# Performance work log

Measured on AMD Instinct MI355X. Metric: run time of the kernel, lower is better.

Reference implementation:

```python
import jax, jax.numpy as jnp
import numpy as np

N_HEAD = 16  # matches init_kwargs
LN_EPS = 1e-5


def setup_inputs() -> dict:
    key = jax.random.key(0)
    k0, k1, k2 = jax.random.split(key, 3)
    S, B, D = 2048, 2, 1024
    N, Dh = N_HEAD, D // N_HEAD
    h = jax.random.normal(k0, (S, B, D), dtype=jnp.float32)
    # causal mask, True = masked; source's dim==3 branch: shape [qlen, klen, batch]
    causal = jnp.triu(jnp.ones((S, S), dtype=bool), k=1)
    attn_mask = jnp.broadcast_to(causal[:, :, None], (S, S, B))
    W_qkv = jax.random.normal(k1, (D, 3 * N * Dh), dtype=jnp.float32) * (1.0 / np.sqrt(D))
    W_o = jax.random.normal(k2, (N * Dh, D), dtype=jnp.float32) * (1.0 / np.sqrt(N * Dh))
    gamma = jnp.ones((D,), dtype=jnp.float32)
    beta = jnp.zeros((D,), dtype=jnp.float32)
    return {"h": h, "attn_mask": attn_mask, "W_qkv": W_qkv, "W_o": W_o,
            "gamma": gamma, "beta": beta}


def reference(h, attn_mask, W_qkv, W_o, gamma, beta):
    # h: [S, B, D] (seq, batch, d_model) -- Transformer-XL layout
    S, B, D = h.shape
    N = N_HEAD
    Dh = W_o.shape[0] // N
    scale = 1.0 / np.sqrt(Dh)

    qkv = h @ W_qkv                                   # [S, B, 3*N*Dh]
    q, k, v = jnp.split(qkv, 3, axis=-1)
    q = q.reshape(S, B, N, Dh)
    k = k.reshape(S, B, N, Dh)
    v = v.reshape(S, B, N, Dh)

    # attention scores: [i, j, b, n]
    score = jnp.einsum('ibnd,jbnd->ijbn', q, k) * scale
    # mask (dim==3 branch of source): attn_mask [i, j, b] -> [i, j, b, 1]
    score = jnp.where(attn_mask[:, :, :, None], -jnp.inf, score)
    prob = jax.nn.softmax(score, axis=1)              # softmax over key axis j

    attn_vec = jnp.einsum('ijbn,jbnd->ibnd', prob, v).reshape(S, B, N * Dh)
    attn_out = attn_vec @ W_o                         # [S, B, D]

    # residual + LayerNorm (biased variance, like torch.nn.LayerNorm)
    x = h + attn_out
    mu = jnp.mean(x, axis=-1, keepdims=True)
    var = jnp.mean(jnp.square(x - mu), axis=-1, keepdims=True)
    out = (x - mu) * jax.lax.rsqrt(var + LN_EPS) * gamma + beta
    return out
```

## Files before the change

kernel.cpp:

```cpp
#include <hip/hip_runtime.h>

typedef unsigned short u16;
typedef unsigned int u32;
typedef __attribute__((ext_vector_type(8))) __bf16 bf16x8;
typedef __attribute__((ext_vector_type(4))) float f32x4;
typedef __attribute__((ext_vector_type(8))) unsigned short u16x8;
typedef __attribute__((ext_vector_type(4))) unsigned short u16x4;
typedef __attribute__((ext_vector_type(2))) unsigned int u32x2;
typedef __attribute__((ext_vector_type(4))) unsigned int u32x4;

#if defined(__has_builtin)
#if __has_builtin(__builtin_amdgcn_permlane32_swap) && __has_builtin(__builtin_amdgcn_permlane16_swap)
#define USE_PERMLANE 1
#endif
#endif
#ifndef USE_PERMLANE
#define USE_PERMLANE 0
#endif

__device__ __forceinline__ u16 f2bf(float f) {
    u32 u = __builtin_bit_cast(u32, f);
    u += 0x7fffu + ((u >> 16) & 1u);
    return (u16)(u >> 16);
}

__device__ __forceinline__ float fexp2(float x) {
#if __has_builtin(__builtin_amdgcn_exp2f)
    return __builtin_amdgcn_exp2f(x);
#else
    return exp2f(x);
#endif
}

__device__ __forceinline__ float frcp(float x) {
#if __has_builtin(__builtin_amdgcn_rcpf)
    return __builtin_amdgcn_rcpf(x);
#else
    return 1.0f / x;
#endif
}

__global__ __launch_bounds__(256) void conv_h_kernel(const float* __restrict__ h,
                                                     u16* __restrict__ hb) {
    int i = blockIdx.x * 256 + threadIdx.x;
    float4 v = ((const float4*)h)[i];
    u16x4 o = { f2bf(v.x), f2bf(v.y), f2bf(v.z), f2bf(v.w) };
    ((u16x4*)hb)[i] = o;
}

__global__ __launch_bounds__(256) void conv_wt_kernel(const float* __restrict__ W,
                                                      u16* __restrict__ Wt,
                                                      int R, int C,
                                                      int scale_rows, float scale) {
    __shared__ float tile[32][33];
    int t = threadIdx.x;
    int r = t >> 3, c4 = (t & 7) * 4;
    int gx = blockIdx.x * 32, gy = blockIdx.y * 32;
    float4 v = *(const float4*)&W[(size_t)(gy + r) * C + gx + c4];
    tile[r][c4 + 0] = v.x; tile[r][c4 + 1] = v.y;
    tile[r][c4 + 2] = v.z; tile[r][c4 + 3] = v.w;
    __syncthreads();
    float sc = (gx + r < scale_rows) ? scale : 1.0f;
    u16x4 o = { f2bf(tile[c4 + 0][r] * sc), f2bf(tile[c4 + 1][r] * sc),
                f2bf(tile[c4 + 2][r] * sc), f2bf(tile[c4 + 3][r] * sc) };
    *(u16x4*)&Wt[(size_t)(gx + r) * R + gy + c4] = o;
}

template <int MODE>
__global__ __launch_bounds__(256) void gemm_bt_kernel(
        const u16* __restrict__ A, const u16* __restrict__ Bt,
        u16* __restrict__ Cb, const float* __restrict__ H, float* __restrict__ X,
        int M, int N, int K) {
    constexpr int LDT = 40;
    __shared__ u16 alds[2][128 * LDT];
    __shared__ u16 blds[2][128 * LDT];
    const int t = threadIdx.x;
    const int lane = t & 63;
    const int wave = t >> 6;
    const int wm = wave >> 1, wn = wave & 1;
    const int m0 = blockIdx.x * 128;
    const int n0 = blockIdx.y * 128;
    const int nk = K >> 5;

    const int srow = t >> 1;
    const int sch = (t & 1) * 2;
    const u16* ga = A + (size_t)(m0 + srow) * K + sch * 8;
    const u16* gb = Bt + (size_t)(n0 + srow) * K + sch * 8;
    const int wo = srow * LDT + sch * 8;

    u16x8 ra0 = *(const u16x8*)(ga);
    u16x8 ra1 = *(const u16x8*)(ga + 8);
    u16x8 rb0 = *(const u16x8*)(gb);
    u16x8 rb1 = *(const u16x8*)(gb + 8);
    *(u16x8*)&alds[0][wo] = ra0;  *(u16x8*)&alds[0][wo + 8] = ra1;
    *(u16x8*)&blds[0][wo] = rb0;  *(u16x8*)&blds[0][wo + 8] = rb1;

    f32x4 acc[4][4] = {};
    const int ko = (lane >> 4) * 8;
    const int arow_base = wm * 64 + (lane & 15);
    const int brow_base = wn * 64 + (lane & 15);

    int cur = 0;
    for (int kt = 0; kt < nk; ++kt) {
        __syncthreads();
        if (kt + 1 < nk) {
            const u16* gan = ga + (kt + 1) * 32;
            const u16* gbn = gb + (kt + 1) * 32;
            ra0 = *(const u16x8*)(gan);
            ra1 = *(const u16x8*)(gan + 8);
            rb0 = *(const u16x8*)(gbn);
            rb1 = *(const u16x8*)(gbn + 8);
        }
        bf16x8 afrag[4], bfrag[4];
#pragma unroll
        for (int m = 0; m < 4; ++m)
            afrag[m] = *(const bf16x8*)&alds[cur][(arow_base + m * 16) * LDT + ko];
#pragma unroll
        for (int n = 0; n < 4; ++n)
            bfrag[n] = *(const bf16x8*)&blds[cur][(brow_base + n * 16) * LDT + ko];
#pragma unroll
        for (int m = 0; m < 4; ++m)
#pragma unroll
            for (int n = 0; n < 4; ++n)
                acc[m][n] = __builtin_amdgcn_mfma_f32_16x16x32_bf16(afrag[m], bfrag[n],
                                                                   acc[m][n], 0, 0, 0);
        if (kt + 1 < nk) {
            *(u16x8*)&alds[cur ^ 1][wo] = ra0;  *(u16x8*)&alds[cur ^ 1][wo + 8] = ra1;
            *(u16x8*)&blds[cur ^ 1][wo] = rb0;  *(u16x8*)&blds[cur ^ 1][wo + 8] = rb1;
        }
        cur ^= 1;
    }

#pragma unroll
    for (int m = 0; m < 4; ++m)
#pragma unroll
        for (int n = 0; n < 4; ++n)
#pragma unroll
            for (int r = 0; r < 4; ++r) {
                int row = m0 + wm * 64 + m * 16 + (lane >> 4) * 4 + r;
                int col = n0 + wn * 64 + n * 16 + (lane & 15);
                size_t idx = (size_t)row * N + col;
                if (MODE == 0) Cb[idx] = f2bf(acc[m][n][r]);
                else           X[idx] = acc[m][n][r] + H[idx];
            }
}

__global__ __launch_bounds__(256) void transpose_v_kernel(const u16* __restrict__ qkvb,
                                                          u16* __restrict__ vt) {
    __shared__ u16 tl[64][72];
    const int t = threadIdx.x;
    const int p = blockIdx.y;
    const int nn = p >> 1, b = p & 1;
    const int s0 = blockIdx.x * 64;
    const int r = t >> 2;
    const int ch = (t & 3) * 2;
    const u16* g = qkvb + ((size_t)(s0 + r) * 2 + b) * 3072 + 2048 + nn * 64;
    *(u16x8*)&tl[r][ch * 8]     = *(const u16x8*)(g + ch * 8);
    *(u16x8*)&tl[r][ch * 8 + 8] = *(const u16x8*)(g + ch * 8 + 8);
    __syncthreads();
    const int dh = t >> 2;
    const int sc = (t & 3) * 2;
    u16* o = vt + ((size_t)p * 64 + dh) * 2048 + s0;
#pragma unroll
    for (int q = 0; q < 2; ++q) {
        int scq = sc + q;
        u16x8 v;
#pragma unroll
        for (int j = 0; j < 8; ++j) v[j] = tl[scq * 8 + j][dh];
        *(u16x8*)(o + scq * 8) = v;
    }
}

__global__ __launch_bounds__(256) void attn_kernel(const u16* __restrict__ qkvb,
                                                   const u16* __restrict__ vt,
                                                   u16* __restrict__ attnb) {
    constexpr int LKT = 72;
    __shared__ u16 klds[2][64 * LKT];
    __shared__ u16 vlds[2][64 * LKT];
#if !USE_PERMLANE
    __shared__ u16 plds[4][16 * LKT];
#endif
    const int t = threadIdx.x;
    const int lane = t & 63;
    const int w = t >> 6;
    const int bid = blockIdx.x;
    const int g = bid >> 5;
    const int sq = g & 7, jq = g >> 3;
    const int qt = (jq == 0) ? (31 - sq) : (jq == 1) ? (16 + sq)
                 : (jq == 2) ? (15 - sq) : sq;
    const int p = bid & 31;
    const int nn = p >> 1, b = p & 1;
    const int i0 = qt * 64;

    const int li = lane & 15;
    const int lg = lane >> 4;

    const int qrow = i0 + w * 16 + li;
    const u16* qg = qkvb + ((size_t)qrow * 2 + b) * 3072 + nn * 64 + lg * 8;
    bf16x8 qa0 = *(const bf16x8*)(qg);
    bf16x8 qa1 = *(const bf16x8*)(qg + 32);

    f32x4 o[4] = {};
    float mrun = -3.0e38f;
    float lrun = 0.f;

    const int srow = t >> 2;
    const int sch = (t & 3) * 2;
    const u16* kg = qkvb + 1024 + nn * 64 + sch * 8;
    const u16* vg = vt + ((size_t)p * 64 + srow) * 2048 + sch * 8;
    const int swo = srow * LKT + sch * 8;

    const int nt = qt + 1;
    u16x8 k0, k1, v0, v1;
    {
        const u16* kgp = kg + ((size_t)srow * 2 + b) * 3072;
        k0 = *(const u16x8*)(kgp);  k1 = *(const u16x8*)(kgp + 8);
        v0 = *(const u16x8*)(vg);   v1 = *(const u16x8*)(vg + 8);
    }
    *(u16x8*)&klds[0][swo] = k0;  *(u16x8*)&klds[0][swo + 8] = k1;
    *(u16x8*)&vlds[0][swo] = v0;  *(u16x8*)&vlds[0][swo + 8] = v1;
    __syncthreads();

    for (int jt = 0; jt < nt; ++jt) {
        const int buf = jt & 1;
        if (jt + 1 < nt) {
            const u16* kgp = kg + ((size_t)(jt * 64 + 64 + srow) * 2 + b) * 3072;
            k0 = *(const u16x8*)(kgp);  k1 = *(const u16x8*)(kgp + 8);
            const u16* vgp = vg + jt * 64 + 64;
            v0 = *(const u16x8*)(vgp);  v1 = *(const u16x8*)(vgp + 8);
        }

        f32x4 st[4];
        __builtin_amdgcn_s_setprio(1);
#pragma unroll
        for (int cf = 0; cf < 4; ++cf) {
            bf16x8 kb0 = *(const bf16x8*)&klds[buf][(cf * 16 + li) * LKT + lg * 8];
            bf16x8 kb1 = *(const bf16x8*)&klds[buf][(cf * 16 + li) * LKT + 32 + lg * 8];
            f32x4 z = {};
            z = __builtin_amdgcn_mfma_f32_16x16x32_bf16(kb0, qa0, z, 0, 0, 0);
            z = __builtin_amdgcn_mfma_f32_16x16x32_bf16(kb1, qa1, z, 0, 0, 0);
            st[cf] = z;
        }
        __builtin_amdgcn_s_setprio(0);

        if (jt == qt) {
            const int it = w * 16 + li;
#pragma unroll
            for (int cf = 0; cf < 4; ++cf)
#pragma unroll
                for (int r = 0; r < 4; ++r) {
                    int jl = cf * 16 + lg * 4 + r;
                    if (jl > it) st[cf][r] = -3.0e38f;
                }
        }

        float mloc = st[0][0];
#pragma unroll
        for (int cf = 0; cf < 4; ++cf)
#pragma unroll
            for (int r = 0; r < 4; ++r) mloc = fmaxf(mloc, st[cf][r]);
        mloc = fmaxf(mloc, __shfl_xor(mloc, 16, 64));
        mloc = fmaxf(mloc, __shfl_xor(mloc, 32, 64));

        if (__any(mloc > mrun + 8.0f)) {
            float mnew = fmaxf(mrun, mloc);
            float alpha = fexp2(mrun - mnew);
            lrun *= alpha;
            mrun = mnew;
#pragma unroll
            for (int r = 0; r < 4; ++r) {
                float ar = __shfl(alpha, lg * 4 + r, 64);
#pragma unroll
                for (int cf = 0; cf < 4; ++cf) o[cf][r] *= ar;
            }
        }

#if USE_PERMLANE
        float rsum = 0.f;
        u32 wv[4][2];
#pragma unroll
        for (int cf = 0; cf < 4; ++cf)
#pragma unroll
            for (int rr = 0; rr < 2; ++rr) {
                float p0 = fexp2(st[cf][2 * rr] - mrun);
                float p1 = fexp2(st[cf][2 * rr + 1] - mrun);
                rsum += p0 + p1;
                u32 wres;
                asm("v_cvt_pk_bf16_f32 %0, %1, %2" : "=v"(wres) : "v"(p0), "v"(p1));
                wv[cf][rr] = wres;
            }
        rsum += __shfl_xor(rsum, 16, 64);
        rsum += __shfl_xor(rsum, 32, 64);
        lrun += rsum;

        __builtin_amdgcn_s_setprio(1);
#pragma unroll
        for (int ks = 0; ks < 2; ++ks) {
            u32x2 sa = __builtin_amdgcn_permlane32_swap(wv[2 * ks][0], wv[2 * ks + 1][0], false, false);
            u32x2 fa = __builtin_amdgcn_permlane16_swap(sa[0], sa[1], false, false);
            u32x2 sb = __builtin_amdgcn_permlane32_swap(wv[2 * ks][1], wv[2 * ks + 1][1], false, false);
            u32x2 fb = __builtin_amdgcn_permlane16_swap(sb[0], sb[1], false, false);
            u32x4 fw = { fa[0], fb[0], fa[1], fb[1] };
            bf16x8 pa = __builtin_bit_cast(bf16x8, fw);
#pragma unroll
            for (int cf = 0; cf < 4; ++cf) {
                bf16x8 vb = *(const bf16x8*)&vlds[buf][(cf * 16 + li) * LKT + ks * 32 + lg * 8];
                o[cf] = __builtin_amdgcn_mfma_f32_16x16x32_bf16(pa, vb, o[cf], 0, 0, 0);
            }
        }
        __builtin_amdgcn_s_setprio(0);
#else
        float rsum = 0.f;
#pragma unroll
        for (int cf = 0; cf < 4; ++cf) {
            u16x4 pw;
#pragma unroll
            for (int r = 0; r < 4; ++r) {
                float pv = fexp2(st[cf][r] - mrun);
                rsum += pv;
                pw[r] = f2bf(pv);
            }
            *(u16x4*)&plds[w][li * LKT + cf * 16 + lg * 4] = pw;
        }
        rsum += __shfl_xor(rsum, 16, 64);
        rsum += __shfl_xor(rsum, 32, 64);
        lrun += rsum;

        asm volatile("s_waitcnt lgkmcnt(0)" ::: "memory");
        __builtin_amdgcn_sched_barrier(0);

#pragma unroll
        for (int ks = 0; ks < 2; ++ks) {
            bf16x8 pa = *(const bf16x8*)&plds[w][li * LKT + ks * 32 + lg * 8];
#pragma unroll
            for (int cf = 0; cf < 4; ++cf) {
                bf16x8 vb = *(const bf16x8*)&vlds[buf][(cf * 16 + li) * LKT + ks * 32 + lg * 8];
                o[cf] = __builtin_amdgcn_mfma_f32_16x16x32_bf16(pa, vb, o[cf], 0, 0, 0);
            }
        }
#endif

        if (jt + 1 < nt) {
            *(u16x8*)&klds[buf ^ 1][swo] = k0;  *(u16x8*)&klds[buf ^ 1][swo + 8] = k1;
            *(u16x8*)&vlds[buf ^ 1][swo] = v0;  *(u16x8*)&vlds[buf ^ 1][swo + 8] = v1;
        }
        __syncthreads();
    }

    float rinv = frcp(lrun);
#pragma unroll
    for (int r = 0; r < 4; ++r) {
        float rv = __shfl(rinv, lg * 4 + r, 64);
        int srowg = i0 + w * 16 + lg * 4 + r;
        u16* og = attnb + ((size_t)srowg * 2 + b) * 1024 + nn * 64;
#pragma unroll
        for (int cf = 0; cf < 4; ++cf)
            og[cf * 16 + li] = f2bf(o[cf][r] * rv);
    }
}

__global__ __launch_bounds__(256) void ln_kernel(const float* __restrict__ X,
                                                 const float* __restrict__ gamma,
                                                 const float* __restrict__ beta,
                                                 float* __restrict__ out) {
    __shared__ float red[8];
    const int t = threadIdx.x;
    const int row = blockIdx.x;
    float4 v = ((const float4*)(X + (size_t)row * 1024))[t];
    float s = v.x + v.y + v.z + v.w;
#pragma unroll
    for (int off = 1; off < 64; off <<= 1) s += __shfl_xor(s, off, 64);
    if ((t & 63) == 0) red[t >> 6] = s;
    __syncthreads();
    float mu = (red[0] + red[1] + red[2] + red[3]) * (1.f / 1024.f);
    float dx = v.x - mu, dy = v.y - mu, dz = v.z - mu, dw = v.w - mu;
    float q = dx * dx + dy * dy + dz * dz + dw * dw;
#pragma unroll
    for (int off = 1; off < 64; off <<= 1) q += __shfl_xor(q, off, 64);
    if ((t & 63) == 0) red[4 + (t >> 6)] = q;
    __syncthreads();
    float var = (red[4] + red[5] + red[6] + red[7]) * (1.f / 1024.f);
    float rs = rsqrtf(var + 1e-5f);
    float4 g = ((const float4*)gamma)[t];
    float4 bt = ((const float4*)beta)[t];
    float4 o;
    o.x = dx * rs * g.x + bt.x;
    o.y = dy * rs * g.y + bt.y;
    o.z = dz * rs * g.z + bt.z;
    o.w = dw * rs * g.w + bt.w;
    ((float4*)(out + (size_t)row * 1024))[t] = o;
}

extern "C" void kernel_launch(void* const* d_in, const int* in_sizes, int n_in,
                              void* d_out, int out_size, void* d_ws, size_t ws_size,
                              hipStream_t stream) {
    const float* h     = (const float*)d_in[0];
    const float* Wqkv  = (const float*)d_in[2];
    const float* Wo    = (const float*)d_in[3];
    const float* gamma = (const float*)d_in[4];
    const float* beta  = (const float*)d_in[5];
    float* out = (float*)d_out;

    char* ws = (char*)d_ws;
    u16*   hb    = (u16*)(ws);
    u16*   wqkvt = (u16*)(ws + 8388608);
    u16*   wot   = (u16*)(ws + 14680064);
    u16*   qkvb  = (u16*)(ws + 16777216);
    u16*   vt    = (u16*)(ws + 41943040);
    u16*   attnb = (u16*)(ws + 50331648);
    float* xbuf  = (float*)(ws + 58720256);

    const float qscale = 0.125f * 1.44269504088896f;

    conv_h_kernel<<<4096, 256, 0, stream>>>(h, hb);
    conv_wt_kernel<<<dim3(96, 32), 256, 0, stream>>>(Wqkv, wqkvt, 1024, 3072, 1024, qscale);
    conv_wt_kernel<<<dim3(32, 32), 256, 0, stream>>>(Wo, wot, 1024, 1024, 0, 1.0f);
    gemm_bt_kernel<0><<<dim3(32, 24), 256, 0, stream>>>(hb, wqkvt, qkvb, nullptr, nullptr,
                                                        4096, 3072, 1024);
    transpose_v_kernel<<<dim3(32, 32), 256, 0, stream>>>(qkvb, vt);
    attn_kernel<<<1024, 256, 0, stream>>>(qkvb, vt, attnb);
    gemm_bt_kernel<1><<<dim3(32, 8), 256, 0, stream>>>(attnb, wot, nullptr, h, xbuf,
                                                       4096, 1024, 1024);
    ln_kernel<<<4096, 256, 0, stream>>>(xbuf, gamma, beta, out);
}
```

Measured before the change: 117.7 us.

## Load K/V fragments directly from global memory, dropping LDS staging and barriers

The attention kernel no longer stages K and V tiles through double-buffered shared memory. Each wave now loads its MFMA operand fragments straight from global memory (L2/L1) every iteration, and the per-iteration __syncthreads is removed. This cuts LDS traffic and block-wide synchronisation, but all four waves now load the same K/V data redundantly. It also loses the software prefetch that overlapped loads with compute, so the load latency is exposed.

```diff
diff --git a/kernel.cpp b/kernel.cpp
--- a/kernel.cpp
+++ b/kernel.cpp
@@ -174,10 +174,8 @@
 __global__ __launch_bounds__(256) void attn_kernel(const u16* __restrict__ qkvb,
                                                    const u16* __restrict__ vt,
                                                    u16* __restrict__ attnb) {
+#if !USE_PERMLANE
     constexpr int LKT = 72;
-    __shared__ u16 klds[2][64 * LKT];
-    __shared__ u16 vlds[2][64 * LKT];
-#if !USE_PERMLANE
     __shared__ u16 plds[4][16 * LKT];
 #endif
     const int t = threadIdx.x;
@@ -200,48 +198,42 @@
     bf16x8 qa0 = *(const bf16x8*)(qg);
     bf16x8 qa1 = *(const bf16x8*)(qg + 32);
 
+    const u16* kfb = qkvb + 1024 + nn * 64 + lg * 8 + ((size_t)li * 2 + b) * 3072;
+    const u16* vfb = vt + ((size_t)(p * 64 + li)) * 2048 + lg * 8;
+
     f32x4 o[4] = {};
     float mrun = -3.0e38f;
     float lrun = 0.f;
 
-    const int srow = t >> 2;
-    const int sch = (t & 3) * 2;
-    const u16* kg = qkvb + 1024 + nn * 64 + sch * 8;
-    const u16* vg = vt + ((size_t)p * 64 + srow) * 2048 + sch * 8;
-    const int swo = srow * LKT + sch * 8;
-
     const int nt = qt + 1;
-    u16x8 k0, k1, v0, v1;
-    {
-        const u16* kgp = kg + ((size_t)srow * 2 + b) * 3072;
-        k0 = *(const u16x8*)(kgp);  k1 = *(const u16x8*)(kgp + 8);
-        v0 = *(const u16x8*)(vg);   v1 = *(const u16x8*)(vg + 8);
-    }
-    *(u16x8*)&klds[0][swo] = k0;  *(u16x8*)&klds[0][swo + 8] = k1;
-    *(u16x8*)&vlds[0][swo] = v0;  *(u16x8*)&vlds[0][swo + 8] = v1;
-    __syncthreads();
-
     for (int jt = 0; jt < nt; ++jt) {
-        const int buf = jt & 1;
-        if (jt + 1 < nt) {
-            const u16* kgp = kg + ((size_t)(jt * 64 + 64 + srow) * 2 + b) * 3072;
-            k0 = *(const u16x8*)(kgp);  k1 = *(const u16x8*)(kgp + 8);
-            const u16* vgp = vg + jt * 64 + 64;
-            v0 = *(const u16x8*)(vgp);  v1 = *(const u16x8*)(vgp + 8);
+        const size_t j0 = (size_t)jt * 64;
+
+        bf16x8 kb[4][2];
+#pragma unroll
+        for (int cf = 0; cf < 4; ++cf) {
+            const u16* kp = kfb + (j0 + cf * 16) * 6144;
+            kb[cf][0] = *(const bf16x8*)(kp);
+            kb[cf][1] = *(const bf16x8*)(kp + 32);
         }
 
         f32x4 st[4];
         __builtin_amdgcn_s_setprio(1);
 #pragma unroll
         for (int cf = 0; cf < 4; ++cf) {
-            bf16x8 kb0 = *(const bf16x8*)&klds[buf][(cf * 16 + li) * LKT + lg * 8];
-            bf16x8 kb1 = *(const bf16x8*)&klds[buf][(cf * 16 + li) * LKT + 32 + lg * 8];
             f32x4 z = {};
-            z = __builtin_amdgcn_mfma_f32_16x16x32_bf16(kb0, qa0, z, 0, 0, 0);
-            z = __builtin_amdgcn_mfma_f32_16x16x32_bf16(kb1, qa1, z, 0, 0, 0);
+            z = __builtin_amdgcn_mfma_f32_16x16x32_bf16(kb[cf][0], qa0, z, 0, 0, 0);
+            z = __builtin_amdgcn_mfma_f32_16x16x32_bf16(kb[cf][1], qa1, z, 0, 0, 0);
             st[cf] = z;
         }
         __builtin_amdgcn_s_setprio(0);
+
+        bf16x8 vbf[2][4];
+#pragma unroll
+        for (int ks = 0; ks < 2; ++ks)
+#pragma unroll
+            for (int cf = 0; cf < 4; ++cf)
+                vbf[ks][cf] = *(const bf16x8*)(vfb + (size_t)cf * 32768 + j0 + ks * 32);
 
         if (jt == qt) {
             const int it = w * 16 + li;
@@ -303,10 +295,8 @@
             u32x4 fw = { fa[0], fb[0], fa[1], fb[1] };
             bf16x8 pa = __builtin_bit_cast(bf16x8, fw);
 #pragma unroll
-            for (int cf = 0; cf < 4; ++cf) {
-                bf16x8 vb = *(const bf16x8*)&vlds[buf][(cf * 16 + li) * LKT + ks * 32 + lg * 8];
-                o[cf] = __builtin_amdgcn_mfma_f32_16x16x32_bf16(pa, vb, o[cf], 0, 0, 0);
-            }
+            for (int cf = 0; cf < 4; ++cf)
+                o[cf] = __builtin_amdgcn_mfma_f32_16x16x32_bf16(pa, vbf[ks][cf], o[cf], 0, 0, 0);
         }
         __builtin_amdgcn_s_setprio(0);
 #else
@@ -333,18 +323,10 @@
         for (int ks = 0; ks < 2; ++ks) {
             bf16x8 pa = *(const bf16x8*)&plds[w][li * LKT + ks * 32 + lg * 8];
 #pragma unroll
-            for (int cf = 0; cf < 4; ++cf) {
-                bf16x8 vb = *(const bf16x8*)&vlds[buf][(cf * 16 + li) * LKT + ks * 32 + lg * 8];
-                o[cf] = __builtin_amdgcn_mfma_f32_16x16x32_bf16(pa, vb, o[cf], 0, 0, 0);
-            }
-        }
-#endif
-
-        if (jt + 1 < nt) {
-            *(u16x8*)&klds[buf ^ 1][swo] = k0;  *(u16x8*)&klds[buf ^ 1][swo + 8] = k1;
-            *(u16x8*)&vlds[buf ^ 1][swo] = v0;  *(u16x8*)&vlds[buf ^ 1][swo + 8] = v1;
-        }
-        __syncthreads();
+            for (int cf = 0; cf < 4; ++cf)
+                o[cf] = __builtin_amdgcn_mfma_f32_16x16x32_bf16(pa, vbf[ks][cf], o[cf], 0, 0, 0);
+        }
+#endif
     }
 
     float rinv = frcp(lrun);
```

Measured after the change: 199.8 us. 69.7% more time.

## Use k-chunk-major LDS layout and XCD-aware block swizzle in GEMM and attention

Applied to the files above, without the earlier changes.

Reorganizes the shared-memory tiles in both the GEMM and attention kernels from padded row-major (stride 40/72) into a k-chunk-major layout, where each 8-element k slice of all rows is stored contiguously. The intent is to get conflict-free 16-byte LDS reads and writes and to shrink LDS use. The GEMM launch also becomes a 1D grid remapped by a modulo-8 swizzle, so neighbouring tiles land on the same XCD and share L2. The remap assumes the tile count divides evenly by 8.

```diff
diff --git a/kernel.cpp b/kernel.cpp
--- a/kernel.cpp
+++ b/kernel.cpp
@@ -71,34 +71,39 @@
         const u16* __restrict__ A, const u16* __restrict__ Bt,
         u16* __restrict__ Cb, const float* __restrict__ H, float* __restrict__ X,
         int M, int N, int K) {
-    constexpr int LDT = 40;
-    __shared__ u16 alds[2][128 * LDT];
-    __shared__ u16 blds[2][128 * LDT];
+    __shared__ u16 alds[2][4096];
+    __shared__ u16 blds[2][4096];
     const int t = threadIdx.x;
     const int lane = t & 63;
     const int wave = t >> 6;
     const int wm = wave >> 1, wn = wave & 1;
-    const int m0 = blockIdx.x * 128;
-    const int n0 = blockIdx.y * 128;
+    const int li = lane & 15, lg = lane >> 4;
+
+    const int mt = M >> 7;
+    const int nwg = mt * (N >> 7);
+    const int lin = blockIdx.x;
+    const int swzb = (lin & 7) * (nwg >> 3) + (lin >> 3);
+    const int m0 = (swzb % mt) * 128;
+    const int n0 = (swzb / mt) * 128;
     const int nk = K >> 5;
 
     const int srow = t >> 1;
     const int sch = (t & 1) * 2;
     const u16* ga = A + (size_t)(m0 + srow) * K + sch * 8;
     const u16* gb = Bt + (size_t)(n0 + srow) * K + sch * 8;
-    const int wo = srow * LDT + sch * 8;
+    const int wo0 = sch * 1024 + srow * 8;
+    const int wo1 = (sch + 1) * 1024 + srow * 8;
 
     u16x8 ra0 = *(const u16x8*)(ga);
     u16x8 ra1 = *(const u16x8*)(ga + 8);
     u16x8 rb0 = *(const u16x8*)(gb);
     u16x8 rb1 = *(const u16x8*)(gb + 8);
-    *(u16x8*)&alds[0][wo] = ra0;  *(u16x8*)&alds[0][wo + 8] = ra1;
-    *(u16x8*)&blds[0][wo] = rb0;  *(u16x8*)&blds[0][wo + 8] = rb1;
+    *(u16x8*)&alds[0][wo0] = ra0;  *(u16x8*)&alds[0][wo1] = ra1;
+    *(u16x8*)&blds[0][wo0] = rb0;  *(u16x8*)&blds[0][wo1] = rb1;
 
     f32x4 acc[4][4] = {};
-    const int ko = (lane >> 4) * 8;
-    const int arow_base = wm * 64 + (lane & 15);
-    const int brow_base = wn * 64 + (lane & 15);
+    const int arow_base = wm * 64 + li;
+    const int brow_base = wn * 64 + li;
 
     int cur = 0;
     for (int kt = 0; kt < nk; ++kt) {
@@ -114,10 +119,10 @@
         bf16x8 afrag[4], bfrag[4];
 #pragma unroll
         for (int m = 0; m < 4; ++m)
-            afrag[m] = *(const bf16x8*)&alds[cur][(arow_base + m * 16) * LDT + ko];
+            afrag[m] = *(const bf16x8*)&alds[cur][lg * 1024 + (arow_base + m * 16) * 8];
 #pragma unroll
         for (int n = 0; n < 4; ++n)
-            bfrag[n] = *(const bf16x8*)&blds[cur][(brow_base + n * 16) * LDT + ko];
+            bfrag[n] = *(const bf16x8*)&blds[cur][lg * 1024 + (brow_base + n * 16) * 8];
 #pragma unroll
         for (int m = 0; m < 4; ++m)
 #pragma unroll
@@ -125,8 +130,8 @@
                 acc[m][n] = __builtin_amdgcn_mfma_f32_16x16x32_bf16(afrag[m], bfrag[n],
                                                                    acc[m][n], 0, 0, 0);
         if (kt + 1 < nk) {
-            *(u16x8*)&alds[cur ^ 1][wo] = ra0;  *(u16x8*)&alds[cur ^ 1][wo + 8] = ra1;
-            *(u16x8*)&blds[cur ^ 1][wo] = rb0;  *(u16x8*)&blds[cur ^ 1][wo + 8] = rb1;
+            *(u16x8*)&alds[cur ^ 1][wo0] = ra0;  *(u16x8*)&alds[cur ^ 1][wo1] = ra1;
+            *(u16x8*)&blds[cur ^ 1][wo0] = rb0;  *(u16x8*)&blds[cur ^ 1][wo1] = rb1;
         }
         cur ^= 1;
     }
@@ -137,8 +142,8 @@
         for (int n = 0; n < 4; ++n)
 #pragma unroll
             for (int r = 0; r < 4; ++r) {
-                int row = m0 + wm * 64 + m * 16 + (lane >> 4) * 4 + r;
-                int col = n0 + wn * 64 + n * 16 + (lane & 15);
+                int row = m0 + wm * 64 + m * 16 + lg * 4 + r;
+                int col = n0 + wn * 64 + n * 16 + li;
                 size_t idx = (size_t)row * N + col;
                 if (MODE == 0) Cb[idx] = f2bf(acc[m][n][r]);
                 else           X[idx] = acc[m][n][r] + H[idx];
@@ -174,11 +179,10 @@
 __global__ __launch_bounds__(256) void attn_kernel(const u16* __restrict__ qkvb,
                                                    const u16* __restrict__ vt,
                                                    u16* __restrict__ attnb) {
-    constexpr int LKT = 72;
-    __shared__ u16 klds[2][64 * LKT];
-    __shared__ u16 vlds[2][64 * LKT];
+    __shared__ u16 klds[2][4096];
+    __shared__ u16 vlds[2][4096];
 #if !USE_PERMLANE
-    __shared__ u16 plds[4][16 * LKT];
+    __shared__ u16 plds[4][16 * 72];
 #endif
     const int t = threadIdx.x;
     const int lane = t & 63;
@@ -208,7 +212,8 @@
     const int sch = (t & 3) * 2;
     const u16* kg = qkvb + 1024 + nn * 64 + sch * 8;
     const u16* vg = vt + ((size_t)p * 64 + srow) * 2048 + sch * 8;
-    const int swo = srow * LKT + sch * 8;
+    const int w0 = sch * 512 + srow * 8;
+    const int w1 = (sch + 1) * 512 + srow * 8;
 
     const int nt = qt + 1;
     u16x8 k0, k1, v0, v1;
@@ -217,8 +222,8 @@
         k0 = *(const u16x8*)(kgp);  k1 = *(const u16x8*)(kgp + 8);
         v0 = *(const u16x8*)(vg);   v1 = *(const u16x8*)(vg + 8);
     }
-    *(u16x8*)&klds[0][swo] = k0;  *(u16x8*)&klds[0][swo + 8] = k1;
-    *(u16x8*)&vlds[0][swo] = v0;  *(u16x8*)&vlds[0][swo + 8] = v1;
+    *(u16x8*)&klds[0][w0] = k0;  *(u16x8*)&klds[0][w1] = k1;
+    *(u16x8*)&vlds[0][w0] = v0;  *(u16x8*)&vlds[0][w1] = v1;
     __syncthreads();
 
     for (int jt = 0; jt < nt; ++jt) {
@@ -234,8 +239,8 @@
         __builtin_amdgcn_s_setprio(1);
 #pragma unroll
         for (int cf = 0; cf < 4; ++cf) {
-            bf16x8 kb0 = *(const bf16x8*)&klds[buf][(cf * 16 + li) * LKT + lg * 8];
-            bf16x8 kb1 = *(const bf16x8*)&klds[buf][(cf * 16 + li) * LKT + 32 + lg * 8];
+            bf16x8 kb0 = *(const bf16x8*)&klds[buf][lg * 512 + (cf * 16 + li) * 8];
+            bf16x8 kb1 = *(const bf16x8*)&klds[buf][(4 + lg) * 512 + (cf * 16 + li) * 8];
             f32x4 z = {};
             z = __builtin_amdgcn_mfma_f32_16x16x32_bf16(kb0, qa0, z, 0, 0, 0);
             z = __builtin_amdgcn_mfma_f32_16x16x32_bf16(kb1, qa1, z, 0, 0, 0);
@@ -304,7 +309,7 @@
             bf16x8 pa = __builtin_bit_cast(bf16x8, fw);
 #pragma unroll
             for (int cf = 0; cf < 4; ++cf) {
-                bf16x8 vb = *(const bf16x8*)&vlds[buf][(cf * 16 + li) * LKT + ks * 32 + lg * 8];
+                bf16x8 vb = *(const bf16x8*)&vlds[buf][(ks * 4 + lg) * 512 + (cf * 16 + li) * 8];
                 o[cf] = __builtin_amdgcn_mfma_f32_16x16x32_bf16(pa, vb, o[cf], 0, 0, 0);
             }
         }
@@ -320,7 +325,7 @@
                 rsum += pv;
                 pw[r] = f2bf(pv);
             }
-            *(u16x4*)&plds[w][li * LKT + cf * 16 + lg * 4] = pw;
+            *(u16x4*)&plds[w][li * 72 + cf * 16 + lg * 4] = pw;
         }
         rsum += __shfl_xor(rsum, 16, 64);
         rsum += __shfl_xor(rsum, 32, 64);
@@ -331,18 +336,18 @@
 
 #pragma unroll
         for (int ks = 0; ks < 2; ++ks) {
-            bf16x8 pa = *(const bf16x8*)&plds[w][li * LKT + ks * 32 + lg * 8];
+            bf16x8 pa = *(const bf16x8*)&plds[w][li * 72 + ks * 32 + lg * 8];
 #pragma unroll
             for (int cf = 0; cf < 4; ++cf) {
-                bf16x8 vb = *(const bf16x8*)&vlds[buf][(cf * 16 + li) * LKT + ks * 32 + lg * 8];
+                bf16x8 vb = *(const bf16x8*)&vlds[buf][(ks * 4 + lg) * 512 + (cf * 16 + li) * 8];
                 o[cf] = __builtin_amdgcn_mfma_f32_16x16x32_bf16(pa, vb, o[cf], 0, 0, 0);
             }
         }
 #endif
 
         if (jt + 1 < nt) {
-            *(u16x8*)&klds[buf ^ 1][swo] = k0;  *(u16x8*)&klds[buf ^ 1][swo + 8] = k1;
-            *(u16x8*)&vlds[buf ^ 1][swo] = v0;  *(u16x8*)&vlds[buf ^ 1][swo + 8] = v1;
+            *(u16x8*)&klds[buf ^ 1][w0] = k0;  *(u16x8*)&klds[buf ^ 1][w1] = k1;
+            *(u16x8*)&vlds[buf ^ 1][w0] = v0;  *(u16x8*)&vlds[buf ^ 1][w1] = v1;
         }
         __syncthreads();
     }
@@ -415,11 +420,11 @@
     conv_h_kernel<<<4096, 256, 0, stream>>>(h, hb);
     conv_wt_kernel<<<dim3(96, 32), 256, 0, stream>>>(Wqkv, wqkvt, 1024, 3072, 1024, qscale);
     conv_wt_kernel<<<dim3(32, 32), 256, 0, stream>>>(Wo, wot, 1024, 1024, 0, 1.0f);
-    gemm_bt_kernel<0><<<dim3(32, 24), 256, 0, stream>>>(hb, wqkvt, qkvb, nullptr, nullptr,
-                                                        4096, 3072, 1024);
+    gemm_bt_kernel<0><<<768, 256, 0, stream>>>(hb, wqkvt, qkvb, nullptr, nullptr,
+                                               4096, 3072, 1024);
     transpose_v_kernel<<<dim3(32, 32), 256, 0, stream>>>(qkvb, vt);
     attn_kernel<<<1024, 256, 0, stream>>>(qkvb, vt, attnb);
-    gemm_bt_kernel<1><<<dim3(32, 8), 256, 0, stream>>>(attnb, wot, nullptr, h, xbuf,
-                                                       4096, 1024, 1024);
+    gemm_bt_kernel<1><<<256, 256, 0, stream>>>(attnb, wot, nullptr, h, xbuf,
+                                               4096, 1024, 1024);
     ln_kernel<<<4096, 256, 0, stream>>>(xbuf, gamma, beta, out);
 }
```

Measured after the change: 121.9 us. +3.5%, slower.

## Split attention key tiles across two wave groups and merge partial softmax

Applied to the files above, without the earlier changes.

The attention block grows to 512 threads, split into two groups of four waves. The groups process alternating key tiles of the same query tile, each with its own double-buffered K/V shared-memory slots, and at the end combine their partial outputs and softmax statistics through shared memory. This halves the serial loop length per block, which shortens the long causal tails. The query-tile schedule becomes a simple longest-first order. In exchange it costs more shared memory and registers per block, an extra merge step, and idle waves when the tile count is odd.

```diff
diff --git a/kernel.cpp b/kernel.cpp
--- a/kernel.cpp
+++ b/kernel.cpp
@@ -171,23 +171,20 @@
     }
 }
 
-__global__ __launch_bounds__(256) void attn_kernel(const u16* __restrict__ qkvb,
+__global__ __launch_bounds__(512) void attn_kernel(const u16* __restrict__ qkvb,
                                                    const u16* __restrict__ vt,
                                                    u16* __restrict__ attnb) {
     constexpr int LKT = 72;
-    __shared__ u16 klds[2][64 * LKT];
-    __shared__ u16 vlds[2][64 * LKT];
+    __shared__ u16 kvs[2][2][2][64 * LKT];
 #if !USE_PERMLANE
-    __shared__ u16 plds[4][16 * LKT];
+    __shared__ u16 plds[8][16 * LKT];
 #endif
     const int t = threadIdx.x;
     const int lane = t & 63;
-    const int w = t >> 6;
+    const int w = (t >> 6) & 3;
+    const int grp = t >> 8;
     const int bid = blockIdx.x;
-    const int g = bid >> 5;
-    const int sq = g & 7, jq = g >> 3;
-    const int qt = (jq == 0) ? (31 - sq) : (jq == 1) ? (16 + sq)
-                 : (jq == 2) ? (15 - sq) : sq;
+    const int qt = 31 - (bid >> 5);
     const int p = bid & 31;
     const int nn = p >> 1, b = p & 1;
     const int i0 = qt * 64;
@@ -204,158 +201,192 @@
     float mrun = -3.0e38f;
     float lrun = 0.f;
 
-    const int srow = t >> 2;
-    const int sch = (t & 3) * 2;
+    const int tg = t & 255;
+    const int srow = tg >> 2;
+    const int sch = (tg & 3) * 2;
     const u16* kg = qkvb + 1024 + nn * 64 + sch * 8;
     const u16* vg = vt + ((size_t)p * 64 + srow) * 2048 + sch * 8;
     const int swo = srow * LKT + sch * 8;
 
     const int nt = qt + 1;
+    const int G = (nt + 1) >> 1;
+
     u16x8 k0, k1, v0, v1;
-    {
-        const u16* kgp = kg + ((size_t)srow * 2 + b) * 3072;
+    if (grp < nt) {
+        const u16* kgp = kg + ((size_t)(grp * 64 + srow) * 2 + b) * 3072;
         k0 = *(const u16x8*)(kgp);  k1 = *(const u16x8*)(kgp + 8);
-        v0 = *(const u16x8*)(vg);   v1 = *(const u16x8*)(vg + 8);
-    }
-    *(u16x8*)&klds[0][swo] = k0;  *(u16x8*)&klds[0][swo + 8] = k1;
-    *(u16x8*)&vlds[0][swo] = v0;  *(u16x8*)&vlds[0][swo + 8] = v1;
-    __syncthreads();
-
-    for (int jt = 0; jt < nt; ++jt) {
-        const int buf = jt & 1;
-        if (jt + 1 < nt) {
-            const u16* kgp = kg + ((size_t)(jt * 64 + 64 + srow) * 2 + b) * 3072;
+        const u16* vgp = vg + grp * 64;
+        v0 = *(const u16x8*)(vgp);  v1 = *(const u16x8*)(vgp + 8);
+        *(u16x8*)&kvs[grp][0][0][swo] = k0;  *(u16x8*)&kvs[grp][0][0][swo + 8] = k1;
+        *(u16x8*)&kvs[grp][0][1][swo] = v0;  *(u16x8*)&kvs[grp][0][1][swo + 8] = v1;
+    }
+    __syncthreads();
+
+    for (int s = 0; s < G; ++s) {
+        const int jt = 2 * s + grp;
+        const int buf = s & 1;
+        const bool active = jt < nt;
+        if (jt + 2 < nt) {
+            const u16* kgp = kg + ((size_t)((jt + 2) * 64 + srow) * 2 + b) * 3072;
             k0 = *(const u16x8*)(kgp);  k1 = *(const u16x8*)(kgp + 8);
-            const u16* vgp = vg + jt * 64 + 64;
+            const u16* vgp = vg + (jt + 2) * 64;
             v0 = *(const u16x8*)(vgp);  v1 = *(const u16x8*)(vgp + 8);
         }
 
-        f32x4 st[4];
-        __builtin_amdgcn_s_setprio(1);
-#pragma unroll
-        for (int cf = 0; cf < 4; ++cf) {
-            bf16x8 kb0 = *(const bf16x8*)&klds[buf][(cf * 16 + li) * LKT + lg * 8];
-            bf16x8 kb1 = *(const bf16x8*)&klds[buf][(cf * 16 + li) * LKT + 32 + lg * 8];
-            f32x4 z = {};
-            z = __builtin_amdgcn_mfma_f32_16x16x32_bf16(kb0, qa0, z, 0, 0, 0);
-            z = __builtin_amdgcn_mfma_f32_16x16x32_bf16(kb1, qa1, z, 0, 0, 0);
-            st[cf] = z;
-        }
-        __builtin_amdgcn_s_setprio(0);
-
-        if (jt == qt) {
-            const int it = w * 16 + li;
+        if (active) {
+            const u16* kl = &kvs[grp][buf][0][0];
+            const u16* vl = &kvs[grp][buf][1][0];
+
+            f32x4 st[4];
+            __builtin_amdgcn_s_setprio(1);
+#pragma unroll
+            for (int cf = 0; cf < 4; ++cf) {
+                bf16x8 kb0 = *(const bf16x8*)&kl[(cf * 16 + li) * LKT + lg * 8];
+                bf16x8 kb1 = *(const bf16x8*)&kl[(cf * 16 + li) * LKT + 32 + lg * 8];
+                f32x4 z = {};
+                z = __builtin_amdgcn_mfma_f32_16x16x32_bf16(kb0, qa0, z, 0, 0, 0);
+                z = __builtin_amdgcn_mfma_f32_16x16x32_bf16(kb1, qa1, z, 0, 0, 0);
+                st[cf] = z;
+            }
+            __builtin_amdgcn_s_setprio(0);
+
+            if (jt == qt) {
+                const int it = w * 16 + li;
+#pragma unroll
+                for (int cf = 0; cf < 4; ++cf)
+#pragma unroll
+                    for (int r = 0; r < 4; ++r) {
+                        int jl = cf * 16 + lg * 4 + r;
+                        if (jl > it) st[cf][r] = -3.0e38f;
+                    }
+            }
+
+            float mloc = st[0][0];
 #pragma unroll
             for (int cf = 0; cf < 4; ++cf)
 #pragma unroll
+                for (int r = 0; r < 4; ++r) mloc = fmaxf(mloc, st[cf][r]);
+            mloc = fmaxf(mloc, __shfl_xor(mloc, 16, 64));
+            mloc = fmaxf(mloc, __shfl_xor(mloc, 32, 64));
+
+            if (__any(mloc > mrun + 8.0f)) {
+                float mnew = fmaxf(mrun, mloc);
+                float alpha = fexp2(mrun - mnew);
+                lrun *= alpha;
+                mrun = mnew;
+#pragma unroll
                 for (int r = 0; r < 4; ++r) {
-                    int jl = cf * 16 + lg * 4 + r;
-                    if (jl > it) st[cf][r] = -3.0e38f;
+                    float ar = __shfl(alpha, lg * 4 + r, 64);
+#pragma unroll
+                    for (int cf = 0; cf < 4; ++cf) o[cf][r] *= ar;
                 }
-        }
-
-        float mloc = st[0][0];
+            }
+
+#if USE_PERMLANE
+            float rsum = 0.f;
+            u32 wv[4][2];
+#pragma unroll
+            for (int cf = 0; cf < 4; ++cf)
+#pragma unroll
+                for (int rr = 0; rr < 2; ++rr) {
+                    float p0 = fexp2(st[cf][2 * rr] - mrun);
+                    float p1 = fexp2(st[cf][2 * rr + 1] - mrun);
+                    rsum += p0 + p1;
+                    u32 wres;
+                    asm("v_cvt_pk_bf16_f32 %0, %1, %2" : "=v"(wres) : "v"(p0), "v"(p1));
+                    wv[cf][rr] = wres;
+                }
+            rsum += __shfl_xor(rsum, 16, 64);
+            rsum += __shfl_xor(rsum, 32, 64);
+            lrun += rsum;
+
+            __builtin_amdgcn_s_setprio(1);
+#pragma unroll
+            for (int ks = 0; ks < 2; ++ks) {
+                u32x2 sa = __builtin_amdgcn_permlane32_swap(wv[2 * ks][0], wv[2 * ks + 1][0], false, false);
+                u32x2 fa = __builtin_amdgcn_permlane16_swap(sa[0], sa[1], false, false);
+                u32x2 sb = __builtin_amdgcn_permlane32_swap(wv[2 * ks][1], wv[2 * ks + 1][1], false, false);
+                u32x2 fb = __builtin_amdgcn_permlane16_swap(sb[0], sb[1], false, false);
+                u32x4 fw = { fa[0], fb[0], fa[1], fb[1] };
+                bf16x8 pa = __builtin_bit_cast(bf16x8, fw);
+#pragma unroll
+                for (int cf = 0; cf < 4; ++cf) {
+                    bf16x8 vb = *(const bf16x8*)&vl[(cf * 16 + li) * LKT + ks * 32 + lg * 8];
+                    o[cf] = __builtin_amdgcn_mfma_f32_16x16x32_bf16(pa, vb, o[cf], 0, 0, 0);
+                }
+            }
+            __builtin_amdgcn_s_setprio(0);
+#else
+            float rsum = 0.f;
+#pragma unroll
+            for (int cf = 0; cf < 4; ++cf) {
+                u16x4 pw;
+#pragma unroll
+                for (int r = 0; r < 4; ++r) {
+                    float pv = fexp2(st[cf][r] - mrun);
+                    rsum += pv;
+                    pw[r] = f2bf(pv);
+                }
+                *(u16x4*)&plds[t >> 6][li * LKT + cf * 16 + lg * 4] = pw;
+            }
+            rsum += __shfl_xor(rsum, 16, 64);
+            rsum += __shfl_xor(rsum, 32, 64);
+            lrun += rsum;
+
+            asm volatile("s_waitcnt lgkmcnt(0)" ::: "memory");
+            __builtin_amdgcn_sched_barrier(0);
+
+#pragma unroll
+            for (int ks = 0; ks < 2; ++ks) {
+                bf16x8 pa = *(const bf16x8*)&plds[t >> 6][li * LKT + ks * 32 + lg * 8];
+#pragma unroll
+                for (int cf = 0; cf < 4; ++cf) {
+                    bf16x8 vb = *(const bf16x8*)&vl[(cf * 16 + li) * LKT + ks * 32 + lg * 8];
+                    o[cf] = __builtin_amdgcn_mfma_f32_16x16x32_bf16(pa, vb, o[cf], 0, 0, 0);
+                }
+            }
+#endif
+        }
+
+        if (jt + 2 < nt) {
+            *(u16x8*)&kvs[grp][buf ^ 1][0][swo] = k0;  *(u16x8*)&kvs[grp][buf ^ 1][0][swo + 8] = k1;
+            *(u16x8*)&kvs[grp][buf ^ 1][1][swo] = v0;  *(u16x8*)&kvs[grp][buf ^ 1][1][swo + 8] = v1;
+        }
+        __syncthreads();
+    }
+
+    float* osc = (float*)&kvs[1][0][0][0];
+    float* msc = osc + 64 * 65;
+    float* lsc = msc + 64;
+    if (grp == 1) {
 #pragma unroll
         for (int cf = 0; cf < 4; ++cf)
 #pragma unroll
-            for (int r = 0; r < 4; ++r) mloc = fmaxf(mloc, st[cf][r]);
-        mloc = fmaxf(mloc, __shfl_xor(mloc, 16, 64));
-        mloc = fmaxf(mloc, __shfl_xor(mloc, 32, 64));
-
-        if (__any(mloc > mrun + 8.0f)) {
-            float mnew = fmaxf(mrun, mloc);
-            float alpha = fexp2(mrun - mnew);
-            lrun *= alpha;
-            mrun = mnew;
-#pragma unroll
-            for (int r = 0; r < 4; ++r) {
-                float ar = __shfl(alpha, lg * 4 + r, 64);
-#pragma unroll
-                for (int cf = 0; cf < 4; ++cf) o[cf][r] *= ar;
-            }
-        }
-
-#if USE_PERMLANE
-        float rsum = 0.f;
-        u32 wv[4][2];
-#pragma unroll
-        for (int cf = 0; cf < 4; ++cf)
-#pragma unroll
-            for (int rr = 0; rr < 2; ++rr) {
-                float p0 = fexp2(st[cf][2 * rr] - mrun);
-                float p1 = fexp2(st[cf][2 * rr + 1] - mrun);
-                rsum += p0 + p1;
-                u32 wres;
-                asm("v_cvt_pk_bf16_f32 %0, %1, %2" : "=v"(wres) : "v"(p0), "v"(p1));
-                wv[cf][rr] = wres;
-            }
-        rsum += __shfl_xor(rsum, 16, 64);
-        rsum += __shfl_xor(rsum, 32, 64);
-        lrun += rsum;
-
-        __builtin_amdgcn_s_setprio(1);
-#pragma unroll
-        for (int ks = 0; ks < 2; ++ks) {
-            u32x2 sa = __builtin_amdgcn_permlane32_swap(wv[2 * ks][0], wv[2 * ks + 1][0], false, false);
-            u32x2 fa = __builtin_amdgcn_permlane16_swap(sa[0], sa[1], false, false);
-            u32x2 sb = __builtin_amdgcn_permlane32_swap(wv[2 * ks][1], wv[2 * ks + 1][1], false, false);
-            u32x2 fb = __builtin_amdgcn_permlane16_swap(sb[0], sb[1], false, false);
-            u32x4 fw = { fa[0], fb[0], fa[1], fb[1] };
-            bf16x8 pa = __builtin_bit_cast(bf16x8, fw);
+            for (int r = 0; r < 4; ++r)
+                osc[(w * 16 + lg * 4 + r) * 65 + cf * 16 + li] = o[cf][r];
+        if (lg == 0) { msc[w * 16 + li] = mrun; lsc[w * 16 + li] = lrun; }
+    }
+    __syncthreads();
+    if (grp == 0) {
+        float mB = msc[w * 16 + li];
+        float lB = lsc[w * 16 + li];
+        float m = fmaxf(mrun, mB);
+        float eA = fexp2(mrun - m);
+        float eB = fexp2(mB - m);
+        float linv = frcp(lrun * eA + lB * eB);
+#pragma unroll
+        for (int r = 0; r < 4; ++r) {
+            float eAr = __shfl(eA, lg * 4 + r, 64);
+            float eBr = __shfl(eB, lg * 4 + r, 64);
+            float rvr = __shfl(linv, lg * 4 + r, 64);
+            int row = i0 + w * 16 + lg * 4 + r;
+            u16* og = attnb + ((size_t)row * 2 + b) * 1024 + nn * 64;
 #pragma unroll
             for (int cf = 0; cf < 4; ++cf) {
-                bf16x8 vb = *(const bf16x8*)&vlds[buf][(cf * 16 + li) * LKT + ks * 32 + lg * 8];
-                o[cf] = __builtin_amdgcn_mfma_f32_16x16x32_bf16(pa, vb, o[cf], 0, 0, 0);
-            }
-        }
-        __builtin_amdgcn_s_setprio(0);
-#else
-        float rsum = 0.f;
-#pragma unroll
-        for (int cf = 0; cf < 4; ++cf) {
-            u16x4 pw;
-#pragma unroll
-            for (int r = 0; r < 4; ++r) {
-                float pv = fexp2(st[cf][r] - mrun);
-                rsum += pv;
-                pw[r] = f2bf(pv);
-            }
-            *(u16x4*)&plds[w][li * LKT + cf * 16 + lg * 4] = pw;
-        }
-        rsum += __shfl_xor(rsum, 16, 64);
-        rsum += __shfl_xor(rsum, 32, 64);
-        lrun += rsum;
-
-        asm volatile("s_waitcnt lgkmcnt(0)" ::: "memory");
-        __builtin_amdgcn_sched_barrier(0);
-
-#pragma unroll
-        for (int ks = 0; ks < 2; ++ks) {
-            bf16x8 pa = *(const bf16x8*)&plds[w][li * LKT + ks * 32 + lg * 8];
-#pragma unroll
-            for (int cf = 0; cf < 4; ++cf) {
-                bf16x8 vb = *(const bf16x8*)&vlds[buf][(cf * 16 + li) * LKT + ks * 32 + lg * 8];
-                o[cf] = __builtin_amdgcn_mfma_f32_16x16x32_bf16(pa, vb, o[cf], 0, 0, 0);
-            }
-        }
-#endif
-
-        if (jt + 1 < nt) {
-            *(u16x8*)&klds[buf ^ 1][swo] = k0;  *(u16x8*)&klds[buf ^ 1][swo + 8] = k1;
-            *(u16x8*)&vlds[buf ^ 1][swo] = v0;  *(u16x8*)&vlds[buf ^ 1][swo + 8] = v1;
-        }
-        __syncthreads();
-    }
-
-    float rinv = frcp(lrun);
-#pragma unroll
-    for (int r = 0; r < 4; ++r) {
-        float rv = __shfl(rinv, lg * 4 + r, 64);
-        int srowg = i0 + w * 16 + lg * 4 + r;
-        u16* og = attnb + ((size_t)srowg * 2 + b) * 1024 + nn * 64;
-#pragma unroll
-        for (int cf = 0; cf < 4; ++cf)
-            og[cf * 16 + li] = f2bf(o[cf][r] * rv);
+                float ob = osc[(w * 16 + lg * 4 + r) * 65 + cf * 16 + li];
+                og[cf * 16 + li] = f2bf((o[cf][r] * eAr + ob * eBr) * rvr);
+            }
+        }
     }
 }
 
@@ -418,7 +449,7 @@
     gemm_bt_kernel<0><<<dim3(32, 24), 256, 0, stream>>>(hb, wqkvt, qkvb, nullptr, nullptr,
                                                         4096, 3072, 1024);
     transpose_v_kernel<<<dim3(32, 32), 256, 0, stream>>>(qkvb, vt);
-    attn_kernel<<<1024, 256, 0, stream>>>(qkvb, vt, attnb);
+    attn_kernel<<<1024, 512, 0, stream>>>(qkvb, vt, attnb);
     gemm_bt_kernel<1><<<dim3(32, 8), 256, 0, stream>>>(attnb, wot, nullptr, h, xbuf,
                                                        4096, 1024, 1024);
     ln_kernel<<<4096, 256, 0, stream>>>(xbuf, gamma, beta, out);
```

After: 117.3 us. About the same (-0.3%).
